# Optimization experiments

Measured on AMD Instinct MI355X. Metric: run time of the kernel, lower is better.

Reference implementation:

```python
import jax, jax.numpy as jnp
import numpy as np

K = 7          # kernel_size
GC = 16        # group_channels (hardcoded in module)
EPS = 1e-5     # BatchNorm eps


def setup_inputs() -> dict:
    key = jax.random.key(0)
    ks = jax.random.split(key, 4)
    B, C, H, W = 4, 256, 56, 56
    Cr = C // 4                      # reduction_ratio = 4
    G = C // GC                      # groups = 16
    return {
        "x": jax.random.normal(ks[0], (B, C, H, W), jnp.float32),
        "conv1_w": jax.random.normal(ks[1], (Cr, C), jnp.float32) * 0.05,
        "bn_gamma": jnp.ones((Cr,), jnp.float32),
        "bn_beta": jnp.zeros((Cr,), jnp.float32),
        "bn_mean": jnp.zeros((Cr,), jnp.float32),
        "bn_var": jnp.ones((Cr,), jnp.float32),
        "conv2_w": jax.random.normal(ks[2], (K * K * G, Cr), jnp.float32) * 0.05,
        "conv2_b": jax.random.normal(ks[3], (K * K * G,), jnp.float32) * 0.05,
    }


def _unfold(x, k):
    # torch nn.Unfold with padding=(k-1)//2, stride=1 -> [B, C, k*k, H, W]
    B, C, H, W = x.shape
    p = (k - 1) // 2
    xp = jnp.pad(x, ((0, 0), (0, 0), (p, p), (p, p)))
    patches = jnp.stack(
        [xp[:, :, i:i + H, j:j + W] for i in range(k) for j in range(k)],
        axis=2,
    )  # (kh, kw) flattened, channel-slowest -> matches torch unfold layout
    return patches


def reference(x, conv1_w, bn_gamma, bn_beta, bn_mean, bn_var, conv2_w, conv2_b):
    B, C, H, W = x.shape
    G = C // GC
    # kernel-generation branch (stride == 1, no avgpool)
    w = jnp.einsum('bchw,oc->bohw', x, conv1_w)                 # conv1 1x1
    inv_std = jax.lax.rsqrt(bn_var + EPS)
    w = (w - bn_mean[None, :, None, None]) * (bn_gamma * inv_std)[None, :, None, None] \
        + bn_beta[None, :, None, None]                           # BN (eval)
    w = jax.nn.relu(w)
    w = jnp.einsum('bchw,oc->bohw', w, conv2_w) + conv2_b[None, :, None, None]
    w = w.reshape(B, G, K * K, H, W)                             # [B,G,K2,H,W]
    # unfold + weighted reduce
    patches = _unfold(x, K).reshape(B, G, GC, K * K, H, W)       # [B,G,gc,K2,H,W]
    out = jnp.einsum('bgkhw,bgckhw->bgchw', w, patches)          # sum over K2
    return out.reshape(B, C, H, W)
```

## Files before the change

kernel.cpp:

```cpp
#include <hip/hip_runtime.h>


#define EPS 1e-5f

typedef __fp16 half2t __attribute__((ext_vector_type(2)));
typedef __fp16 half4t __attribute__((ext_vector_type(4)));
typedef __fp16 half8t __attribute__((ext_vector_type(8)));
typedef float floatx4 __attribute__((ext_vector_type(4)));

__device__ inline half8t pack8(float4 u0, float4 u1, float s) {
    half8t a;
    half2t q;
    q = __builtin_amdgcn_cvt_pkrtz(u0.x * s, u0.y * s); a[0] = q[0]; a[1] = q[1];
    q = __builtin_amdgcn_cvt_pkrtz(u0.z * s, u0.w * s); a[2] = q[0]; a[3] = q[1];
    q = __builtin_amdgcn_cvt_pkrtz(u1.x * s, u1.y * s); a[4] = q[0]; a[5] = q[1];
    q = __builtin_amdgcn_cvt_pkrtz(u1.z * s, u1.w * s); a[6] = q[0]; a[7] = q[1];
    return a;
}

__global__ __launch_bounds__(256, 4) void k1_conv1(
    const float* __restrict__ x, const float* __restrict__ w1,
    const float* __restrict__ gamma, const float* __restrict__ beta,
    const float* __restrict__ mean, const float* __restrict__ var,
    __fp16* __restrict__ mid)
{
    __shared__ __align__(16) __fp16 lxB[32 * 72];
    const int t    = threadIdx.x;
    const int b    = blockIdx.y;
    const int p0   = blockIdx.x * 32;
    const int lane = t & 63, wvid = t >> 6;
    const int mrow = lane & 15, quad = lane >> 4;

    const int orow = wvid * 16 + mrow;
    const float s = gamma[orow] * rsqrtf(var[orow] + EPS);
    half8t A[4][2];
#pragma unroll
    for (int ch = 0; ch < 4; ++ch)
#pragma unroll
        for (int h = 0; h < 2; ++h) {
            const float* src = &w1[orow * 256 + ch * 64 + h * 32 + quad * 8];
            A[ch][h] = pack8(*(const float4*)src, *(const float4*)(src + 4), s);
        }

    floatx4 acc[2] = {};
    const int c2 = t & 31, pxq = t >> 5;
    for (int ch = 0; ch < 4; ++ch) {
        const float* r0 = &x[(size_t)(b * 256 + ch * 64 + 2 * c2) * 3136 + p0 + pxq * 4];
        const float* r1 = r0 + 3136;
        float4 a0 = *(const float4*)r0;
        float4 b0 = *(const float4*)r1;
        const float* f0 = (const float*)&a0;
        const float* f1 = (const float*)&b0;
#pragma unroll
        for (int j = 0; j < 4; ++j) {
            half2t q = __builtin_amdgcn_cvt_pkrtz(f0[j], f1[j]);
            *(half2t*)&lxB[(pxq * 4 + j) * 72 + 2 * c2] = q;
        }
        __syncthreads();
#pragma unroll
        for (int pt = 0; pt < 2; ++pt) {
            half8t bf0 = *(const half8t*)&lxB[(pt * 16 + mrow) * 72 + quad * 8];
            half8t bf1 = *(const half8t*)&lxB[(pt * 16 + mrow) * 72 + quad * 8 + 32];
            acc[pt] = __builtin_amdgcn_mfma_f32_16x16x32_f16(A[ch][0], bf0, acc[pt], 0, 0, 0);
            acc[pt] = __builtin_amdgcn_mfma_f32_16x16x32_f16(A[ch][1], bf1, acc[pt], 0, 0, 0);
        }
        __syncthreads();
    }
    float bb[4];
#pragma unroll
    for (int i = 0; i < 4; ++i) {
        int o = wvid * 16 + quad * 4 + i;
        float so = gamma[o] * rsqrtf(var[o] + EPS);
        bb[i] = beta[o] - mean[o] * so;
    }
#pragma unroll
    for (int pt = 0; pt < 2; ++pt)
#pragma unroll
        for (int i = 0; i < 4; ++i) {
            float v = fmaxf(acc[pt][i] + bb[i], 0.f);
            lxB[(pt * 16 + mrow) * 72 + wvid * 16 + quad * 4 + i] = (__fp16)v;
        }
    __syncthreads();
    {
        int px = t >> 3, o8 = t & 7;
        *(half8t*)&mid[(size_t)(b * 3136 + p0 + px) * 64 + o8 * 8] =
            *(const half8t*)&lxB[px * 72 + o8 * 8];
    }
}

__global__ __launch_bounds__(128, 3) void k2_fused(
    const float* __restrict__ x, const __fp16* __restrict__ mid,
    const float* __restrict__ cw, const float* __restrict__ cb,
    float* __restrict__ out)
{
    __shared__ __align__(16) unsigned char smem[28960];
    __fp16* lmid = (__fp16*)smem;
    __fp16* lxh  = (__fp16*)smem;

    const int t  = threadIdx.x;
    const int b  = blockIdx.z;
    const int gq = blockIdx.y;
    const int th = blockIdx.x / 7, tw = blockIdx.x % 7;
    const int h0 = th * 8, w0 = tw * 8;
    const int lane = t & 63, wvid = t >> 6;
    const int mrow = lane & 15, quad = lane >> 4;
    const int g = gq * 2 + wvid;
    __fp16* lw2h = (__fp16*)(smem + 14848 + wvid * 7056);

    half4t hr[14];
#pragma unroll
    for (int i = 0; i < 14; ++i) {
        int s = t + i * 128;
        int ch = s / 56, r = s % 56;
        int row = r >> 2, cq = r & 3;
        int gh = h0 + row - 3;
        int gwb = w0 - 4 + cq * 4;
        bool ok = (gh >= 0) & (gh < 56) & (gwb >= 0) & (gwb <= 52);
        int ghc = min(max(gh, 0), 55);
        int gwc = min(max(gwb, 0), 52);
        float4 ld = *(const float4*)&x[(size_t)(b * 256 + gq * 32 + ch) * 3136 +
                                       ghc * 56 + gwc];
        if (!ok) ld = make_float4(0.f, 0.f, 0.f, 0.f);
        half2t p0 = __builtin_amdgcn_cvt_pkrtz(ld.x, ld.y);
        half2t p1 = __builtin_amdgcn_cvt_pkrtz(ld.z, ld.w);
        half4t h; h[0] = p0[0]; h[1] = p0[1]; h[2] = p1[0]; h[3] = p1[1];
        hr[i] = h;
    }

#pragma unroll
    for (int i = 0; i < 4; ++i) {
        int s  = t + i * 128;
        int px = s >> 3, c8 = s & 7;
        int pix = (h0 + (px >> 3)) * 56 + w0 + (px & 7);
        *(half8t*)&lmid[px * 72 + c8 * 8] =
            *(const half8t*)&mid[(size_t)(b * 3136 + pix) * 64 + c8 * 8];
    }
    __syncthreads();

    {
        half8t bf[4][2];
#pragma unroll
        for (int pt = 0; pt < 4; ++pt) {
            bf[pt][0] = *(const half8t*)&lmid[(pt * 16 + mrow) * 72 + quad * 8];
            bf[pt][1] = *(const half8t*)&lmid[(pt * 16 + mrow) * 72 + quad * 8 + 32];
        }
#pragma unroll
        for (int mc = 0; mc < 4; ++mc) {
            int krow = mc * 16 + mrow;
            half8t a0 = {}, a1 = {};
            if (krow < 49) {
                const float* src = &cw[(size_t)(g * 49 + krow) * 64 + quad * 8];
                a0 = pack8(*(const float4*)src,        *(const float4*)(src + 4),  1.f);
                a1 = pack8(*(const float4*)(src + 32), *(const float4*)(src + 36), 1.f);
            }
#pragma unroll
            for (int pt = 0; pt < 4; ++pt) {
                floatx4 acc = {0.f, 0.f, 0.f, 0.f};
                acc = __builtin_amdgcn_mfma_f32_16x16x32_f16(a0, bf[pt][0], acc, 0, 0, 0);
                acc = __builtin_amdgcn_mfma_f32_16x16x32_f16(a1, bf[pt][1], acc, 0, 0, 0);
                int px = pt * 16 + mrow;
#pragma unroll
                for (int i = 0; i < 4; ++i) {
                    int ko = mc * 16 + quad * 4 + i;
                    if (ko < 49)
                        lw2h[ko * 72 + px] = (__fp16)(acc[i] + cb[g * 49 + ko]);
                }
            }
        }
    }
    __syncthreads();

#pragma unroll
    for (int i = 0; i < 14; ++i) {
        int s = t + i * 128;
        int ch = s / 56, r = s % 56;
        int row = r >> 2, cq = r & 3;
        *(half4t*)&lxh[ch * 232 + row * 16 + cq * 4] = hr[i];
    }
    __syncthreads();

    const int cc  = lane >> 4;
    const int pxt = lane & 15;
    const int sh  = pxt >> 1, sw4 = (pxt & 1) * 4;
    const int chb = wvid * 16 + cc * 4;
    float acc[4][4] = {};
#pragma unroll
    for (int kh = 0; kh < 7; ++kh) {
        const int row = sh + kh;
        half4t xq[4][3];
#pragma unroll
        for (int i = 0; i < 4; ++i)
#pragma unroll
            for (int q = 0; q < 3; ++q)
                xq[i][q] = *(const half4t*)&lxh[(chb + i) * 232 + row * 16 + sw4 + q * 4];
#pragma unroll
        for (int kw = 0; kw < 7; ++kw) {
            half4t wq = *(const half4t*)&lw2h[(kh * 7 + kw) * 72 + pxt * 4];
#pragma unroll
            for (int j = 0; j < 4; ++j) {
                const int o = 1 + kw + j;
#pragma unroll
                for (int i = 0; i < 4; ++i)
                    acc[i][j] = fmaf((float)wq[j], (float)xq[i][o >> 2][o & 3],
                                     acc[i][j]);
            }
        }
    }
#pragma unroll
    for (int i = 0; i < 4; ++i) {
        *(float4*)&out[(size_t)(b * 256 + g * 16 + cc * 4 + i) * 3136 +
                       (h0 + sh) * 56 + w0 + sw4] =
            make_float4(acc[i][0], acc[i][1], acc[i][2], acc[i][3]);
    }
}

extern "C" void kernel_launch(void* const* d_in, const int* in_sizes, int n_in,
                              void* d_out, int out_size, void* d_ws, size_t ws_size,
                              hipStream_t stream) {
    const float* x     = (const float*)d_in[0];
    const float* w1    = (const float*)d_in[1];
    const float* gamma = (const float*)d_in[2];
    const float* beta  = (const float*)d_in[3];
    const float* mean  = (const float*)d_in[4];
    const float* var   = (const float*)d_in[5];
    const float* cw    = (const float*)d_in[6];
    const float* cb    = (const float*)d_in[7];
    float* out = (float*)d_out;

    __fp16* mid = (__fp16*)d_ws;

    k1_conv1<<<dim3(98, 4), 256, 0, stream>>>(x, w1, gamma, beta, mean, var, mid);
    k2_fused<<<dim3(49, 8, 4), 128, 0, stream>>>(x, mid, cw, cb, out);
}
```

Before: 124.5 us.

## Split k2 work to one group per block with smaller LDS and padded strides

Each k2 block now handles a single group of 16 channels instead of two, so the grid doubles in y. The two waves split both the conv2 MFMA pixel tiles and the channels of the weighted reduce. This lowers per-block LDS and registers, allowing more resident blocks (launch bounds 5), and changes the LDS strides (284/20, 68) to reduce bank conflicts. The cost is that the mid tile is loaded and the halo of x is fetched by twice as many blocks.

```diff
diff --git a/kernel.cpp b/kernel.cpp
--- a/kernel.cpp
+++ b/kernel.cpp
@@ -88,28 +88,27 @@
     }
 }
 
-__global__ __launch_bounds__(128, 3) void k2_fused(
+__global__ __launch_bounds__(128, 5) void k2_fused(
     const float* __restrict__ x, const __fp16* __restrict__ mid,
     const float* __restrict__ cw, const float* __restrict__ cb,
     float* __restrict__ out)
 {
-    __shared__ __align__(16) unsigned char smem[28960];
+    __shared__ __align__(16) unsigned char smem[15880];
     __fp16* lmid = (__fp16*)smem;
     __fp16* lxh  = (__fp16*)smem;
+    __fp16* lw2  = (__fp16*)(smem + 9216);
 
     const int t  = threadIdx.x;
     const int b  = blockIdx.z;
-    const int gq = blockIdx.y;
+    const int g  = blockIdx.y;
     const int th = blockIdx.x / 7, tw = blockIdx.x % 7;
     const int h0 = th * 8, w0 = tw * 8;
     const int lane = t & 63, wvid = t >> 6;
     const int mrow = lane & 15, quad = lane >> 4;
-    const int g = gq * 2 + wvid;
-    __fp16* lw2h = (__fp16*)(smem + 14848 + wvid * 7056);
-
-    half4t hr[14];
-#pragma unroll
-    for (int i = 0; i < 14; ++i) {
+
+    half4t hr[7];
+#pragma unroll
+    for (int i = 0; i < 7; ++i) {
         int s = t + i * 128;
         int ch = s / 56, r = s % 56;
         int row = r >> 2, cq = r & 3;
@@ -118,7 +117,7 @@
         bool ok = (gh >= 0) & (gh < 56) & (gwb >= 0) & (gwb <= 52);
         int ghc = min(max(gh, 0), 55);
         int gwc = min(max(gwb, 0), 52);
-        float4 ld = *(const float4*)&x[(size_t)(b * 256 + gq * 32 + ch) * 3136 +
+        float4 ld = *(const float4*)&x[(size_t)(b * 256 + g * 16 + ch) * 3136 +
                                        ghc * 56 + gwc];
         if (!ok) ld = make_float4(0.f, 0.f, 0.f, 0.f);
         half2t p0 = __builtin_amdgcn_cvt_pkrtz(ld.x, ld.y);
@@ -138,11 +137,12 @@
     __syncthreads();
 
     {
-        half8t bf[4][2];
-#pragma unroll
-        for (int pt = 0; pt < 4; ++pt) {
-            bf[pt][0] = *(const half8t*)&lmid[(pt * 16 + mrow) * 72 + quad * 8];
-            bf[pt][1] = *(const half8t*)&lmid[(pt * 16 + mrow) * 72 + quad * 8 + 32];
+        half8t bf[2][2];
+#pragma unroll
+        for (int p2 = 0; p2 < 2; ++p2) {
+            int pt = wvid * 2 + p2;
+            bf[p2][0] = *(const half8t*)&lmid[(pt * 16 + mrow) * 72 + quad * 8];
+            bf[p2][1] = *(const half8t*)&lmid[(pt * 16 + mrow) * 72 + quad * 8 + 32];
         }
 #pragma unroll
         for (int mc = 0; mc < 4; ++mc) {
@@ -154,16 +154,16 @@
                 a1 = pack8(*(const float4*)(src + 32), *(const float4*)(src + 36), 1.f);
             }
 #pragma unroll
-            for (int pt = 0; pt < 4; ++pt) {
+            for (int p2 = 0; p2 < 2; ++p2) {
                 floatx4 acc = {0.f, 0.f, 0.f, 0.f};
-                acc = __builtin_amdgcn_mfma_f32_16x16x32_f16(a0, bf[pt][0], acc, 0, 0, 0);
-                acc = __builtin_amdgcn_mfma_f32_16x16x32_f16(a1, bf[pt][1], acc, 0, 0, 0);
-                int px = pt * 16 + mrow;
+                acc = __builtin_amdgcn_mfma_f32_16x16x32_f16(a0, bf[p2][0], acc, 0, 0, 0);
+                acc = __builtin_amdgcn_mfma_f32_16x16x32_f16(a1, bf[p2][1], acc, 0, 0, 0);
+                int px = (wvid * 2 + p2) * 16 + mrow;
 #pragma unroll
                 for (int i = 0; i < 4; ++i) {
                     int ko = mc * 16 + quad * 4 + i;
                     if (ko < 49)
-                        lw2h[ko * 72 + px] = (__fp16)(acc[i] + cb[g * 49 + ko]);
+                        lw2[ko * 68 + px] = (__fp16)(acc[i] + cb[g * 49 + ko]);
                 }
             }
         }
@@ -171,44 +171,44 @@
     __syncthreads();
 
 #pragma unroll
-    for (int i = 0; i < 14; ++i) {
+    for (int i = 0; i < 7; ++i) {
         int s = t + i * 128;
         int ch = s / 56, r = s % 56;
         int row = r >> 2, cq = r & 3;
-        *(half4t*)&lxh[ch * 232 + row * 16 + cq * 4] = hr[i];
-    }
-    __syncthreads();
-
-    const int cc  = lane >> 4;
+        *(half4t*)&lxh[ch * 284 + row * 20 + cq * 4] = hr[i];
+    }
+    __syncthreads();
+
+    const int cp  = lane >> 4;
     const int pxt = lane & 15;
     const int sh  = pxt >> 1, sw4 = (pxt & 1) * 4;
-    const int chb = wvid * 16 + cc * 4;
-    float acc[4][4] = {};
+    const int chb = wvid * 8 + cp * 2;
+    float acc[2][4] = {};
 #pragma unroll
     for (int kh = 0; kh < 7; ++kh) {
         const int row = sh + kh;
-        half4t xq[4][3];
-#pragma unroll
-        for (int i = 0; i < 4; ++i)
+        half4t xq[2][3];
+#pragma unroll
+        for (int i = 0; i < 2; ++i)
 #pragma unroll
             for (int q = 0; q < 3; ++q)
-                xq[i][q] = *(const half4t*)&lxh[(chb + i) * 232 + row * 16 + sw4 + q * 4];
+                xq[i][q] = *(const half4t*)&lxh[(chb + i) * 284 + row * 20 + sw4 + q * 4];
 #pragma unroll
         for (int kw = 0; kw < 7; ++kw) {
-            half4t wq = *(const half4t*)&lw2h[(kh * 7 + kw) * 72 + pxt * 4];
+            half4t wq = *(const half4t*)&lw2[(kh * 7 + kw) * 68 + pxt * 4];
 #pragma unroll
             for (int j = 0; j < 4; ++j) {
                 const int o = 1 + kw + j;
 #pragma unroll
-                for (int i = 0; i < 4; ++i)
+                for (int i = 0; i < 2; ++i)
                     acc[i][j] = fmaf((float)wq[j], (float)xq[i][o >> 2][o & 3],
                                      acc[i][j]);
             }
         }
     }
 #pragma unroll
-    for (int i = 0; i < 4; ++i) {
-        *(float4*)&out[(size_t)(b * 256 + g * 16 + cc * 4 + i) * 3136 +
+    for (int i = 0; i < 2; ++i) {
+        *(float4*)&out[(size_t)(b * 256 + g * 16 + chb + i) * 3136 +
                        (h0 + sh) * 56 + w0 + sw4] =
             make_float4(acc[i][0], acc[i][1], acc[i][2], acc[i][3]);
     }
@@ -230,5 +230,5 @@
     __fp16* mid = (__fp16*)d_ws;
 
     k1_conv1<<<dim3(98, 4), 256, 0, stream>>>(x, w1, gamma, beta, mean, var, mid);
-    k2_fused<<<dim3(49, 8, 4), 128, 0, stream>>>(x, mid, cw, cb, out);
-}
+    k2_fused<<<dim3(49, 16, 4), 128, 0, stream>>>(x, mid, cw, cb, out);
+}
```

Measured after the change: 170.8 us. +37.1%, slower.
